# Kernel tuning notes

Hardware: AMD Instinct MI355X
Metric: run time of the kernel (lower is better)

## Reference

```python
import jax, jax.numpy as jnp
import numpy as np


def setup_inputs() -> dict:
    key = jax.random.key(0)
    k1, k2 = jax.random.split(key)
    n, d, num_classes = 262144, 128, 512
    inputs = jax.random.normal(k1, (n, d), dtype=jnp.float32)
    targets = jax.random.randint(k2, (n,), 0, num_classes)
    return {"inputs": inputs, "targets": targets, "num_classes": num_classes}


def reference(inputs, targets, num_classes):
    beta = 0.1
    eps = 1e-12  # torch F.normalize default eps (norm clamped to min eps)
    # L2-normalize features
    x = inputs / jnp.maximum(jnp.linalg.norm(inputs, axis=1, keepdims=True), eps)  # [n, d]

    # Per-class centers: mean of normalized features, then L2-normalize, detached.
    ones = jnp.ones((x.shape[0],), dtype=x.dtype)
    counts = jax.ops.segment_sum(ones, targets, num_segments=num_classes)          # [C]
    csum = jax.ops.segment_sum(x, targets, num_segments=num_classes)               # [C, d]
    cmean = csum / jnp.maximum(counts, 1.0)[:, None]
    centers = cmean / jnp.maximum(jnp.linalg.norm(cmean, axis=1, keepdims=True), eps)
    centers = jax.lax.stop_gradient(centers)  # .detach() in original

    # Numerator logit: center of own class dotted with own feature
    pos = jnp.sum(centers[targets] * x, axis=1) / beta                             # [n]
    # Denominator: sum of exp over all *present* classes (original only builds
    # centers for pids that appear in the batch)
    scores = jnp.exp(centers @ x.T / beta)                                         # [C, n]
    present = counts > 0
    denom = jnp.sum(jnp.where(present[:, None], scores, 0.0), axis=0)              # [n]
    return -jnp.mean(pos - jnp.log(denom))
```

## Files before the change

kernel.cpp:

```cpp
#include <hip/hip_runtime.h>
#include <stdint.h>

#define NROWS 262144
#define DDIM 128
#define NCLS 512
#define NHB 64
constexpr float INV_BETA = 10.0f;
constexpr float EXP2_SCALE = 14.426950408889634f;

typedef __bf16 v8bf __attribute__((ext_vector_type(8)));
typedef float v4f __attribute__((ext_vector_type(4)));

__device__ inline unsigned short f2bf(float f) {
    uint32_t u = __builtin_bit_cast(uint32_t, f);
    u += 0x7FFFu + ((u >> 16) & 1u);
    return (unsigned short)(u >> 16);
}
__device__ inline float bflo(uint32_t u) { return __builtin_bit_cast(float, u << 16); }
__device__ inline float bfhi(uint32_t u) { return __builtin_bit_cast(float, u & 0xFFFF0000u); }

#define GLL16(gsrc, ldst)                                                        \
    __builtin_amdgcn_global_load_lds(                                            \
        (const __attribute__((address_space(1))) void*)(uintptr_t)(gsrc),        \
        (__attribute__((address_space(3))) void*)(uintptr_t)(ldst), 16, 0, 0)

__global__ __launch_bounds__(256) void k1_normalize(
    const float* __restrict__ in, const int* __restrict__ tgt,
    unsigned short* __restrict__ xb, int* __restrict__ bh) {
    __shared__ int h[NCLS];
    int t = threadIdx.x;
    if (blockIdx.x >= 8192) {
        int b = blockIdx.x - 8192;
        for (int i = t; i < NCLS; i += 256) h[i] = 0;
        __syncthreads();
        int base = b * (NROWS / NHB);
        for (int i = base + t; i < base + NROWS / NHB; i += 256)
            atomicAdd(&h[tgt[i]], 1);
        __syncthreads();
        for (int i = t; i < NCLS; i += 256)
            bh[b * NCLS + i] = h[i];
        return;
    }
    int w = t >> 6;
    int half = (t & 63) >> 5;
    int lane32 = t & 31;
    int hw = blockIdx.x * 8 + w * 2 + half;
    int r0 = hw * 4;
    float4 v[4];
#pragma unroll
    for (int j = 0; j < 4; ++j)
        v[j] = *reinterpret_cast<const float4*>(in + (size_t)(r0 + j) * DDIM + lane32 * 4);
    float s[4];
#pragma unroll
    for (int j = 0; j < 4; ++j)
        s[j] = v[j].x * v[j].x + v[j].y * v[j].y + v[j].z * v[j].z + v[j].w * v[j].w;
#pragma unroll
    for (int off = 1; off < 32; off <<= 1) {
#pragma unroll
        for (int j = 0; j < 4; ++j) s[j] += __shfl_xor(s[j], off);
    }
#pragma unroll
    for (int j = 0; j < 4; ++j) {
        float iv = rsqrtf(fmaxf(s[j], 1e-24f));
        ushort4 o;
        o.x = f2bf(v[j].x * iv); o.y = f2bf(v[j].y * iv);
        o.z = f2bf(v[j].z * iv); o.w = f2bf(v[j].w * iv);
        *reinterpret_cast<ushort4*>(xb + (size_t)(r0 + j) * DDIM + lane32 * 4) = o;
    }
}

__global__ __launch_bounds__(512) void k_prefix(
    const int* __restrict__ bh, int* __restrict__ counts, int* __restrict__ offs,
    int* __restrict__ base, float* __restrict__ nabsG, float* __restrict__ out) {
    __shared__ int sc[NCLS];
    __shared__ int za;
    int t = threadIdx.x;
    int cnt = 0;
#pragma unroll 8
    for (int b = 0; b < NHB; ++b) cnt += bh[b * NCLS + t];
    counts[t] = cnt;
    sc[t] = cnt;
    if (t == 0) za = 0;
    __syncthreads();
    for (int off = 1; off < NCLS; off <<= 1) {
        int v = (t >= off) ? sc[t - off] : 0;
        __syncthreads();
        sc[t] += v;
        __syncthreads();
    }
    int excl = sc[t] - cnt;
    offs[t] = excl;
    if (cnt == 0) atomicAdd(&za, 1);
    int run = excl;
    for (int b = 0; b < NHB; ++b) {
        base[b * NCLS + t] = run;
        run += bh[b * NCLS + t];
    }
    __syncthreads();
    if (t == 0) { *nabsG = (float)za; *out = 0.0f; }
}

__global__ __launch_bounds__(256) void k_scatter(
    const int* __restrict__ tgt, const int* __restrict__ base, int* __restrict__ ridx) {
    __shared__ int cur[NCLS];
    int t = threadIdx.x;
    int b = blockIdx.x;
    cur[t] = base[b * NCLS + t];
    cur[t + 256] = base[b * NCLS + t + 256];
    __syncthreads();
    int r0 = b * (NROWS / NHB);
    for (int i = t; i < NROWS / NHB; i += 256) {
        int row = r0 + i;
        int c = tgt[row];
        int pos = atomicAdd(&cur[c], 1);
        ridx[pos] = row;
    }
}

__device__ inline void centers_gather(
    const uint32_t* __restrict__ xb32, const int* __restrict__ ridx,
    int start, int lo, int hi, int l, float& a0, float& a1) {
    int i = lo;
    for (; i + 16 <= hi; i += 16) {
        int id[16]; uint32_t v[16];
#pragma unroll
        for (int j = 0; j < 16; ++j) id[j] = ridx[start + i + j];
#pragma unroll
        for (int j = 0; j < 16; ++j) v[j] = xb32[(size_t)id[j] * 64 + l];
#pragma unroll
        for (int j = 0; j < 16; ++j) { a0 += bflo(v[j]); a1 += bfhi(v[j]); }
    }
    for (; i < hi; ++i) {
        uint32_t v = xb32[(size_t)ridx[start + i] * 64 + l];
        a0 += bflo(v); a1 += bfhi(v);
    }
}

__global__ __launch_bounds__(512) void k_centers(
    const unsigned short* __restrict__ xb, const int* __restrict__ ridx,
    const int* __restrict__ counts, const int* __restrict__ offs,
    unsigned short* __restrict__ cen, float* __restrict__ out) {
    __shared__ float2 sP[8][64];
    int t = threadIdx.x, w = t >> 6, l = t & 63;
    int cl = blockIdx.x;
    int cnt = counts[cl], start = offs[cl];
    float a0 = 0.0f, a1 = 0.0f;
    int per = (cnt + 7) >> 3;
    int lo = w * per, hi = min(cnt, lo + per);
    centers_gather((const uint32_t*)xb, ridx, start, lo, hi, l, a0, a1);
    sP[w][l] = make_float2(a0, a1);
    __syncthreads();
    if (w == 0) {
        float c0 = 0.0f, c1 = 0.0f;
#pragma unroll
        for (int q = 0; q < 8; ++q) { c0 += sP[q][l].x; c1 += sP[q][l].y; }
        float fc = fmaxf((float)cnt, 1.0f);
        c0 /= fc; c1 /= fc;
        float ss = c0 * c0 + c1 * c1;
        for (int off = 1; off < 64; off <<= 1) ss += __shfl_xor(ss, off);
        float inv = EXP2_SCALE / fmaxf(sqrtf(ss), 1e-12f);
        ushort2 o;
        o.x = f2bf(c0 * inv); o.y = f2bf(c1 * inv);
        *reinterpret_cast<ushort2*>(cen + (size_t)cl * DDIM + l * 2) = o;
        if (l == 0)
            atomicAdd(out, -(float)cnt * sqrtf(ss) * (INV_BETA / (float)NROWS));
    }
}

__global__ __launch_bounds__(1024) void k4_loss(
    const unsigned short* __restrict__ xb, const unsigned short* __restrict__ cen,
    const float* __restrict__ nabsG, float* __restrict__ out) {
    extern __shared__ char lds[];
    char* cenL = lds;
    float* wsum = (float*)(lds + 131072);
    int t = threadIdx.x, w = t >> 6, l = t & 63;
    int lm = l & 15, lk = l >> 4;
    float nabs = *nabsG;

    int s0 = blockIdx.x * 1024 + w * 64;
    const char* xB = (const char*)xb;
    v8bf bfr[4][4];
#pragma unroll
    for (int n = 0; n < 4; ++n)
#pragma unroll
        for (int kc = 0; kc < 4; ++kc)
            bfr[n][kc] = *reinterpret_cast<const v8bf*>(
                xB + (size_t)(s0 + n * 16 + lm) * 256 + kc * 64 + lk * 16);

    const char* cB = (const char*)cen;
#pragma unroll
    for (int i = 0; i < 8; ++i) {
        int chunk = w * 8 + i;
        int m = chunk >> 2, kc = chunk & 3;
        int src = (m * 16 + lm) * 256 + kc * 64 + lk * 16;
        GLL16(cB + src, cenL + chunk * 1024);
    }
    asm volatile("s_waitcnt vmcnt(0)" ::: "memory");
    __syncthreads();

    float den[4] = {0.0f, 0.0f, 0.0f, 0.0f};
    for (int m = 0; m < 32; ++m) {
        v8bf a[4];
#pragma unroll
        for (int kc = 0; kc < 4; ++kc)
            a[kc] = *reinterpret_cast<const v8bf*>(cenL + m * 4096 + kc * 1024 + l * 16);
        v4f acc[4];
        v4f zero = {0.0f, 0.0f, 0.0f, 0.0f};
#pragma unroll
        for (int n = 0; n < 4; ++n) acc[n] = zero;
#pragma unroll
        for (int kc = 0; kc < 4; ++kc)
#pragma unroll
            for (int n = 0; n < 4; ++n)
                acc[n] = __builtin_amdgcn_mfma_f32_16x16x32_bf16(a[kc], bfr[n][kc], acc[n], 0, 0, 0);
#pragma unroll
        for (int n = 0; n < 4; ++n)
#pragma unroll
            for (int rr = 0; rr < 4; ++rr)
                den[n] += __builtin_amdgcn_exp2f(acc[n][rr]);
    }

    float lossAcc = 0.0f;
#pragma unroll
    for (int n = 0; n < 4; ++n) {
        float d = den[n];
        d += __shfl_xor(d, 16);
        d += __shfl_xor(d, 32);
        if (l < 16) lossAcc += __logf(d - nabs);
    }
#pragma unroll
    for (int off = 1; off < 64; off <<= 1) lossAcc += __shfl_xor(lossAcc, off);
    if (l == 0) wsum[w] = lossAcc;
    __syncthreads();
    if (t == 0) {
        float s = 0.0f;
#pragma unroll
        for (int q = 0; q < 16; ++q) s += wsum[q];
        atomicAdd(out, s * (1.0f / NROWS));
    }
}

extern "C" void kernel_launch(void* const* d_in, const int* in_sizes, int n_in,
                              void* d_out, int out_size, void* d_ws, size_t ws_size,
                              hipStream_t stream) {
    const float* in = (const float*)d_in[0];
    const int* tgt = (const int*)d_in[1];
    float* out = (float*)d_out;
    char* ws = (char*)d_ws;
    unsigned short* xb = (unsigned short*)(ws);
    int* counts = (int*)(ws + 67108864);
    int* offs = (int*)(ws + 67110912);
    float* nabsG = (float*)(ws + 67112960);
    unsigned short* cen = (unsigned short*)(ws + 67115264);
    int* ridx = (int*)(ws + 67246336);
    int* bh = (int*)(ws + 68294912);
    int* base = (int*)(ws + 68557056);

    (void)hipFuncSetAttribute((const void*)k4_loss,
                              hipFuncAttributeMaxDynamicSharedMemorySize, 131136);

    hipLaunchKernelGGL(k1_normalize, dim3(8192 + NHB), dim3(256), 0, stream, in, tgt, xb, bh);
    hipLaunchKernelGGL(k_prefix, dim3(1), dim3(512), 0, stream, bh, counts, offs, base, nabsG, out);
    hipLaunchKernelGGL(k_scatter, dim3(NHB), dim3(256), 0, stream, tgt, base, ridx);
    hipLaunchKernelGGL(k_centers, dim3(NCLS), dim3(512), 0, stream, xb, ridx, counts, offs, cen, out);
    hipLaunchKernelGGL(k4_loss, dim3(256), dim3(1024), 131136, stream, xb, cen, nabsG, out);
}
```

Measured before the change: 109.7 us.

## Fuse prefix scan into scatter kernel and split exp accumulators

After: 116.1 us. 5.8% more time.

```diff
diff --git a/kernel.cpp b/kernel.cpp
--- a/kernel.cpp
+++ b/kernel.cpp
@@ -69,16 +69,21 @@
     }
 }
 
-__global__ __launch_bounds__(512) void k_prefix(
-    const int* __restrict__ bh, int* __restrict__ counts, int* __restrict__ offs,
-    int* __restrict__ base, float* __restrict__ nabsG, float* __restrict__ out) {
+__global__ __launch_bounds__(512) void k_scatter(
+    const int* __restrict__ bh, const int* __restrict__ tgt,
+    int* __restrict__ counts, int* __restrict__ offs, int* __restrict__ ridx,
+    float* __restrict__ nabsG, float* __restrict__ out) {
     __shared__ int sc[NCLS];
+    __shared__ int cur[NCLS];
     __shared__ int za;
     int t = threadIdx.x;
+    int b = blockIdx.x;
+    int arr[NHB];
+#pragma unroll
+    for (int bb = 0; bb < NHB; ++bb) arr[bb] = bh[bb * NCLS + t];
     int cnt = 0;
-#pragma unroll 8
-    for (int b = 0; b < NHB; ++b) cnt += bh[b * NCLS + t];
-    counts[t] = cnt;
+#pragma unroll
+    for (int bb = 0; bb < NHB; ++bb) cnt += arr[bb];
     sc[t] = cnt;
     if (t == 0) za = 0;
     __syncthreads();
@@ -89,27 +94,18 @@
         __syncthreads();
     }
     int excl = sc[t] - cnt;
-    offs[t] = excl;
-    if (cnt == 0) atomicAdd(&za, 1);
-    int run = excl;
-    for (int b = 0; b < NHB; ++b) {
-        base[b * NCLS + t] = run;
-        run += bh[b * NCLS + t];
-    }
-    __syncthreads();
-    if (t == 0) { *nabsG = (float)za; *out = 0.0f; }
-}
-
-__global__ __launch_bounds__(256) void k_scatter(
-    const int* __restrict__ tgt, const int* __restrict__ base, int* __restrict__ ridx) {
-    __shared__ int cur[NCLS];
-    int t = threadIdx.x;
-    int b = blockIdx.x;
-    cur[t] = base[b * NCLS + t];
-    cur[t + 256] = base[b * NCLS + t + 256];
-    __syncthreads();
+    int myBase = excl;
+    for (int bb = 0; bb < b; ++bb) myBase += arr[bb];
+    cur[t] = myBase;
+    if (b == 0) {
+        counts[t] = cnt;
+        offs[t] = excl;
+        if (cnt == 0) atomicAdd(&za, 1);
+    }
+    __syncthreads();
+    if (b == 0 && t == 0) { *nabsG = (float)za; *out = 0.0f; }
     int r0 = b * (NROWS / NHB);
-    for (int i = t; i < NROWS / NHB; i += 256) {
+    for (int i = t; i < NROWS / NHB; i += 512) {
         int row = r0 + i;
         int c = tgt[row];
         int pos = atomicAdd(&cur[c], 1);
@@ -198,7 +194,7 @@
     asm volatile("s_waitcnt vmcnt(0)" ::: "memory");
     __syncthreads();
 
-    float den[4] = {0.0f, 0.0f, 0.0f, 0.0f};
+    float den[8] = {0.0f, 0.0f, 0.0f, 0.0f, 0.0f, 0.0f, 0.0f, 0.0f};
     for (int m = 0; m < 32; ++m) {
         v8bf a[4];
 #pragma unroll
@@ -217,13 +213,13 @@
         for (int n = 0; n < 4; ++n)
 #pragma unroll
             for (int rr = 0; rr < 4; ++rr)
-                den[n] += __builtin_amdgcn_exp2f(acc[n][rr]);
+                den[n + ((rr & 1) << 2)] += __builtin_amdgcn_exp2f(acc[n][rr]);
     }
 
     float lossAcc = 0.0f;
 #pragma unroll
     for (int n = 0; n < 4; ++n) {
-        float d = den[n];
+        float d = den[n] + den[n + 4];
         d += __shfl_xor(d, 16);
         d += __shfl_xor(d, 32);
         if (l < 16) lossAcc += __logf(d - nabs);
@@ -256,12 +252,12 @@
     int* bh = (int*)(ws + 68294912);
     int* base = (int*)(ws + 68557056);
 
+    (void)base;
     (void)hipFuncSetAttribute((const void*)k4_loss,
                               hipFuncAttributeMaxDynamicSharedMemorySize, 131136);
 
     hipLaunchKernelGGL(k1_normalize, dim3(8192 + NHB), dim3(256), 0, stream, in, tgt, xb, bh);
-    hipLaunchKernelGGL(k_prefix, dim3(1), dim3(512), 0, stream, bh, counts, offs, base, nabsG, out);
-    hipLaunchKernelGGL(k_scatter, dim3(NHB), dim3(256), 0, stream, tgt, base, ridx);
+    hipLaunchKernelGGL(k_scatter, dim3(NHB), dim3(512), 0, stream, bh, tgt, counts, offs, ridx, nabsG, out);
     hipLaunchKernelGGL(k_centers, dim3(NCLS), dim3(512), 0, stream, xb, ridx, counts, offs, cen, out);
     hipLaunchKernelGGL(k4_loss, dim3(256), dim3(1024), 131136, stream, xb, cen, nabsG, out);
 }
```
